# Kernel optimization log

Measured on AMD Instinct MI355X. Metric: run time of the kernel, lower is better.

Reference implementation:

```python
import jax, jax.numpy as jnp
import numpy as np

B, T, D, H, C = 64, 256, 512, 1024, 1000

def setup_inputs() -> dict:
    key = jax.random.key(0)
    ks = jax.random.split(key, 6)
    s = 1.0 / np.sqrt(H)  # torch nn.RNN init scale
    return {
        "x": jax.random.normal(ks[0], (B, T, D), dtype=jnp.float32),
        "w_ih0": jax.random.normal(ks[1], (H, D), dtype=jnp.float32) * s,
        "w_hh0": jax.random.normal(ks[2], (H, H), dtype=jnp.float32) * s,
        "w_ih1": jax.random.normal(ks[3], (H, H), dtype=jnp.float32) * s,
        "w_hh1": jax.random.normal(ks[4], (H, H), dtype=jnp.float32) * s,
        "w_fc": jax.random.normal(ks[5], (C, H), dtype=jnp.float32) * s,
    }

def _rnn_layer(inp, w_ih, w_hh):
    # inp: [B, T, Din]; ReLU RNN, no bias (matches nn.RNN(nonlinearity='relu', bias=False))
    xs = jnp.einsum('btd,hd->tbh', inp, w_ih)  # precompute input projections for all steps
    h0 = jnp.zeros((inp.shape[0], w_hh.shape[0]), dtype=inp.dtype)
    def step(h, x_t):
        h = jax.nn.relu(x_t + h @ w_hh.T)
        return h, h
    _, ys = jax.lax.scan(step, h0, xs)  # ys: [T, B, H]
    return jnp.swapaxes(ys, 0, 1)  # [B, T, H]

def reference(x, w_ih0, w_hh0, w_ih1, w_hh1, w_fc):
    h1 = _rnn_layer(x, w_ih0, w_hh0)
    h2 = _rnn_layer(h1, w_ih1, w_hh1)
    # fc on last timestep, no bias
    return h2[:, -1, :] @ w_fc.T  # [B, C]
```

## Files before the change

### kernel.cpp

```cpp
#include <hip/hip_runtime.h>

#define T_STEPS 256
#define BATCH   64
#define HID     1024
#define DIN     512
#define NCLS    1000
#define NBLK    128
#define HSZ     (BATCH * HID)

typedef __attribute__((ext_vector_type(8))) short  short8;
typedef __attribute__((ext_vector_type(4))) float  f32x4;

__device__ __forceinline__ unsigned short rne_bf16(float f) {
    unsigned int u = __builtin_bit_cast(unsigned int, f);
    u += 0x7FFFu + ((u >> 16) & 1u);
    return (unsigned short)(u >> 16);
}
__device__ __forceinline__ float bf16_to_f(unsigned short h) {
    unsigned int u = ((unsigned int)h) << 16;
    return __builtin_bit_cast(float, u);
}

#define MFMA(a, b, c) __builtin_amdgcn_mfma_f32_16x16x32_bf16((a), (b), (c), 0, 0, 0)

__device__ __forceinline__ void grid_bar(int* cnt, int* gen, int bid, int tid, int p) {
    __syncthreads();
    if (tid == 0) {
        __threadfence();
        __hip_atomic_fetch_add(&cnt[(bid & 7) * 32], 1,
                               __ATOMIC_RELAXED, __HIP_MEMORY_SCOPE_AGENT);
        if (bid == 0) {
            const int target = NBLK * (p + 1);
            for (long it = 0; it < 1000000L; ++it) {
                int s = 0;
#pragma unroll
                for (int i = 0; i < 8; ++i)
                    s += __hip_atomic_load(&cnt[i * 32], __ATOMIC_RELAXED,
                                           __HIP_MEMORY_SCOPE_AGENT);
                if (s >= target) break;
                __builtin_amdgcn_s_sleep(1);
            }
            __threadfence();
            __hip_atomic_store(gen, p + 1, __ATOMIC_RELAXED, __HIP_MEMORY_SCOPE_AGENT);
        } else {
            for (long it = 0; it < 1000000L; ++it) {
                if (__hip_atomic_load(gen, __ATOMIC_RELAXED,
                                      __HIP_MEMORY_SCOPE_AGENT) >= p + 1)
                    break;
                __builtin_amdgcn_s_sleep(1);
            }
            __threadfence();
        }
    }
    __syncthreads();
}

__device__ __forceinline__ void reduce_store(const float* red, int tid,
                                             int mbase, int nbase,
                                             unsigned short* ohi, unsigned short* olo,
                                             float* of, const float* xp) {
    const int m = tid >> 4;
    const int n = (tid * 2) & 31;
    float s0, s1;
    if (xp) {
        float2 xi = *(const float2*)(xp + (size_t)(mbase + m) * HID + nbase + n);
        s0 = xi.x; s1 = xi.y;
    } else { s0 = 0.f; s1 = 0.f; }
#pragma unroll
    for (int ww = 0; ww < 8; ++ww) {
        const float* rp = red + ww * 1088 + m * 34 + n;
        s0 += rp[0];
        s1 += rp[1];
    }
    const float v0 = fmaxf(s0, 0.f), v1 = fmaxf(s1, 0.f);
    const unsigned short h0 = rne_bf16(v0), h1 = rne_bf16(v1);
    const unsigned int hp = (unsigned int)h0 | ((unsigned int)h1 << 16);
    const unsigned int lp = (unsigned int)rne_bf16(v0 - bf16_to_f(h0)) |
                            ((unsigned int)rne_bf16(v1 - bf16_to_f(h1)) << 16);
    const size_t o = (size_t)(mbase + m) * HID + nbase + n;
    *(unsigned int*)(ohi + o) = hp;
    *(unsigned int*)(olo + o) = lp;
    if (of) { float2 f2; f2.x = v0; f2.y = v1; *(float2*)(of + o) = f2; }
}

__global__ __launch_bounds__(512, 2)
void rnn_mfma(const float* __restrict__ xproj,
              const unsigned short* __restrict__ whh0h, const unsigned short* __restrict__ whh0l,
              const unsigned short* __restrict__ wih1h, const unsigned short* __restrict__ wih1l,
              const unsigned short* __restrict__ whh1h, const unsigned short* __restrict__ whh1l,
              unsigned short* h1hi, unsigned short* h1lo,
              unsigned short* h2hi, unsigned short* h2lo,
              float* h2f, int* bar) {
    __shared__ float red[8 * 1088];

    const int bid   = blockIdx.x;
    const int z     = bid >> 6;
    const int r     = bid & 63;
    const int nbase = (r >> 1) * 32;
    const int mbase = (r & 1) * 32;
    const int tid   = threadIdx.x;
    const int w     = tid >> 6;
    const int lane  = tid & 63;
    const int l15   = lane & 15;
    const int kq    = (lane >> 4) * 8;

    int* cnt = bar;
    int* gen = bar + 256;

    if (z == 0) {
        short8 WH[2][4], WL[2][4];
        const int kb = w * 128;
#pragma unroll
        for (int c = 0; c < 4; ++c)
#pragma unroll
            for (int nt = 0; nt < 2; ++nt) {
                const size_t o = (size_t)(nbase + nt * 16 + l15) * HID + kb + c * 32 + kq;
                WH[nt][c] = *(const short8*)(whh0h + o);
                WL[nt][c] = *(const short8*)(whh0l + o);
            }
        for (int p = 0; p <= T_STEPS; ++p) {
            if (p < T_STEPS) {
                f32x4 acc[2][2] = {};
                const unsigned short* hch = h1hi + (size_t)(p & 1) * HSZ;
                const unsigned short* hcl = h1lo + (size_t)(p & 1) * HSZ;
#pragma unroll
                for (int c = 0; c < 4; ++c) {
                    short8 ah[2], al[2];
#pragma unroll
                    for (int mt = 0; mt < 2; ++mt) {
                        const size_t o = (size_t)(mbase + mt * 16 + l15) * HID + kb + c * 32 + kq;
                        ah[mt] = *(const short8*)(hch + o);
                        al[mt] = *(const short8*)(hcl + o);
                    }
#pragma unroll
                    for (int mt = 0; mt < 2; ++mt)
#pragma unroll
                        for (int nt = 0; nt < 2; ++nt) {
                            acc[mt][nt] = MFMA(ah[mt], WH[nt][c], acc[mt][nt]);
                            acc[mt][nt] = MFMA(al[mt], WH[nt][c], acc[mt][nt]);
                            acc[mt][nt] = MFMA(ah[mt], WL[nt][c], acc[mt][nt]);
                        }
                }
#pragma unroll
                for (int mt = 0; mt < 2; ++mt)
#pragma unroll
                    for (int nt = 0; nt < 2; ++nt)
#pragma unroll
                        for (int i = 0; i < 4; ++i)
                            red[w * 1088 + (mt * 16 + (lane >> 4) * 4 + i) * 34 +
                                nt * 16 + l15] = acc[mt][nt][i];
                __syncthreads();
                const size_t ob = (size_t)((p + 1) & 1) * HSZ;
                reduce_store(red, tid, mbase, nbase, h1hi + ob, h1lo + ob, nullptr,
                             xproj + (size_t)p * BATCH * HID);
            }
            grid_bar(cnt, gen, bid, tid, p);
        }
    } else {
        short8 WH[2][8], WL[2][8];
        const unsigned short* ph = (w < 4) ? wih1h : whh1h;
        const unsigned short* pl = (w < 4) ? wih1l : whh1l;
        const int kb = (w & 3) * 256;
#pragma unroll
        for (int c = 0; c < 8; ++c)
#pragma unroll
            for (int nt = 0; nt < 2; ++nt) {
                const size_t o = (size_t)(nbase + nt * 16 + l15) * HID + kb + c * 32 + kq;
                WH[nt][c] = *(const short8*)(ph + o);
                WL[nt][c] = *(const short8*)(pl + o);
            }
        for (int p = 0; p <= T_STEPS; ++p) {
            if (p >= 1) {
                f32x4 acc[2][2] = {};
                const unsigned short* ash = (w < 4) ? h1hi + (size_t)(p & 1) * HSZ
                                                    : h2hi + (size_t)((p - 1) & 1) * HSZ;
                const unsigned short* asl = (w < 4) ? h1lo + (size_t)(p & 1) * HSZ
                                                    : h2lo + (size_t)((p - 1) & 1) * HSZ;
#pragma unroll
                for (int c = 0; c < 8; ++c) {
                    short8 ah[2], al[2];
#pragma unroll
                    for (int mt = 0; mt < 2; ++mt) {
                        const size_t o = (size_t)(mbase + mt * 16 + l15) * HID + kb + c * 32 + kq;
                        ah[mt] = *(const short8*)(ash + o);
                        al[mt] = *(const short8*)(asl + o);
                    }
#pragma unroll
                    for (int mt = 0; mt < 2; ++mt)
#pragma unroll
                        for (int nt = 0; nt < 2; ++nt) {
                            acc[mt][nt] = MFMA(ah[mt], WH[nt][c], acc[mt][nt]);
                            acc[mt][nt] = MFMA(al[mt], WH[nt][c], acc[mt][nt]);
                            acc[mt][nt] = MFMA(ah[mt], WL[nt][c], acc[mt][nt]);
                        }
                }
#pragma unroll
                for (int mt = 0; mt < 2; ++mt)
#pragma unroll
                    for (int nt = 0; nt < 2; ++nt)
#pragma unroll
                        for (int i = 0; i < 4; ++i)
                            red[w * 1088 + (mt * 16 + (lane >> 4) * 4 + i) * 34 +
                                nt * 16 + l15] = acc[mt][nt][i];
                __syncthreads();
                const size_t ob = (size_t)(p & 1) * HSZ;
                reduce_store(red, tid, mbase, nbase, h2hi + ob, h2lo + ob,
                             (p == T_STEPS) ? h2f : nullptr, nullptr);
            }
            grid_bar(cnt, gen, bid, tid, p);
        }
    }
}

__global__ __launch_bounds__(512)
void xproj_gemm(const float* __restrict__ x,
                const unsigned short* __restrict__ wh,
                const unsigned short* __restrict__ wl,
                float* __restrict__ xproj) {
    const int t    = blockIdx.x;
    const int nq   = blockIdx.y;
    const int w    = threadIdx.x >> 6;
    const int lane = threadIdx.x & 63;
    const int l15  = lane & 15;
    const int kq   = (lane >> 4) * 8;
    const int n0   = nq * 256 + w * 32;

    f32x4 acc[4][2] = {};
    for (int c = 0; c < 16; ++c) {
        const int k = c * 32 + kq;
        short8 wfh[2], wfl[2];
#pragma unroll
        for (int nt = 0; nt < 2; ++nt) {
            const size_t o = (size_t)(n0 + nt * 16 + l15) * DIN + k;
            wfh[nt] = *(const short8*)(wh + o);
            wfl[nt] = *(const short8*)(wl + o);
        }
#pragma unroll
        for (int mt = 0; mt < 4; ++mt) {
            const float* xr = x + ((size_t)(mt * 16 + l15) * T_STEPS + t) * DIN + k;
            float4 a0 = *(const float4*)xr;
            float4 a1 = *(const float4*)(xr + 4);
            float f[8] = {a0.x, a0.y, a0.z, a0.w, a1.x, a1.y, a1.z, a1.w};
            short8 ah, al;
#pragma unroll
            for (int i = 0; i < 8; ++i) {
                unsigned short h = rne_bf16(f[i]);
                ah[i] = (short)h;
                al[i] = (short)rne_bf16(f[i] - bf16_to_f(h));
            }
#pragma unroll
            for (int nt = 0; nt < 2; ++nt) {
                acc[mt][nt] = MFMA(ah, wfh[nt], acc[mt][nt]);
                acc[mt][nt] = MFMA(al, wfh[nt], acc[mt][nt]);
                acc[mt][nt] = MFMA(ah, wfl[nt], acc[mt][nt]);
            }
        }
    }
    float* op = xproj + (size_t)t * BATCH * HID;
#pragma unroll
    for (int mt = 0; mt < 4; ++mt)
#pragma unroll
        for (int nt = 0; nt < 2; ++nt)
#pragma unroll
            for (int i = 0; i < 4; ++i) {
                const int m = mt * 16 + (lane >> 4) * 4 + i;
                const int n = n0 + nt * 16 + l15;
                op[(size_t)m * HID + n] = acc[mt][nt][i];
            }
}

__global__ void split_w(const float* __restrict__ src,
                        unsigned short* __restrict__ hi,
                        unsigned short* __restrict__ lo, int n) {
    int i = blockIdx.x * 256 + threadIdx.x;
    if (i < n) {
        float v = src[i];
        unsigned short h = rne_bf16(v);
        hi[i] = h;
        lo[i] = rne_bf16(v - bf16_to_f(h));
    }
}

__global__ void zero_kernel(int* __restrict__ p, int n) {
    int i = blockIdx.x * 256 + threadIdx.x;
    if (i < n) p[i] = 0;
}

__global__ void fc_kernel(const float* __restrict__ h2,
                          const float* __restrict__ w_fc,
                          float* __restrict__ out) {
    __shared__ float hs[HID];
    const int b = blockIdx.x;
    for (int i = threadIdx.x; i < HID; i += 256) hs[i] = h2[(size_t)b * HID + i];
    __syncthreads();
    const int c = blockIdx.y * 256 + threadIdx.x;
    if (c < NCLS) {
        const float* w = w_fc + (size_t)c * HID;
        float s = 0.f;
        for (int k = 0; k < HID; k += 4) {
            float4 wv = *(const float4*)(w + k);
            s += wv.x * hs[k] + wv.y * hs[k + 1] + wv.z * hs[k + 2] + wv.w * hs[k + 3];
        }
        out[(size_t)b * NCLS + c] = s;
    }
}

extern "C" void kernel_launch(void* const* d_in, const int* in_sizes, int n_in,
                              void* d_out, int out_size, void* d_ws, size_t ws_size,
                              hipStream_t stream) {
    const float* x     = (const float*)d_in[0];
    const float* w_ih0 = (const float*)d_in[1];
    const float* w_hh0 = (const float*)d_in[2];
    const float* w_ih1 = (const float*)d_in[3];
    const float* w_hh1 = (const float*)d_in[4];
    const float* w_fc  = (const float*)d_in[5];
    float* out = (float*)d_out;

    char* ws = (char*)d_ws;
    size_t off = 0;
    auto alloc = [&](size_t bytes) { char* p = ws + off; off += bytes; return p; };
    float*          xproj = (float*)alloc((size_t)T_STEPS * BATCH * HID * 4);
    unsigned short* wih0h = (unsigned short*)alloc((size_t)DIN * HID * 2);
    unsigned short* wih0l = (unsigned short*)alloc((size_t)DIN * HID * 2);
    unsigned short* whh0h = (unsigned short*)alloc((size_t)HID * HID * 2);
    unsigned short* whh0l = (unsigned short*)alloc((size_t)HID * HID * 2);
    unsigned short* wih1h = (unsigned short*)alloc((size_t)HID * HID * 2);
    unsigned short* wih1l = (unsigned short*)alloc((size_t)HID * HID * 2);
    unsigned short* whh1h = (unsigned short*)alloc((size_t)HID * HID * 2);
    unsigned short* whh1l = (unsigned short*)alloc((size_t)HID * HID * 2);
    unsigned short* h1hi  = (unsigned short*)alloc(2 * HSZ * 2);
    unsigned short* h1lo  = (unsigned short*)alloc(2 * HSZ * 2);
    unsigned short* h2hi  = (unsigned short*)alloc(2 * HSZ * 2);
    unsigned short* h2lo  = (unsigned short*)alloc(2 * HSZ * 2);
    float*          h2f   = (float*)alloc(HSZ * 4);
    int*            bar   = (int*)alloc(4096);

    split_w<<<(DIN * HID + 255) / 256, 256, 0, stream>>>(w_ih0, wih0h, wih0l, DIN * HID);
    split_w<<<(HID * HID + 255) / 256, 256, 0, stream>>>(w_hh0, whh0h, whh0l, HID * HID);
    split_w<<<(HID * HID + 255) / 256, 256, 0, stream>>>(w_ih1, wih1h, wih1l, HID * HID);
    split_w<<<(HID * HID + 255) / 256, 256, 0, stream>>>(w_hh1, whh1h, whh1l, HID * HID);

    xproj_gemm<<<dim3(T_STEPS, 4), 512, 0, stream>>>(x, wih0h, wih0l, xproj);

    const int nzero = (4 * (2 * HSZ * 2) + HSZ * 4 + 4096) / 4;
    zero_kernel<<<(nzero + 255) / 256, 256, 0, stream>>>((int*)h1hi, nzero);

    rnn_mfma<<<NBLK, 512, 0, stream>>>(xproj,
                                       whh0h, whh0l,
                                       wih1h, wih1l, whh1h, whh1l,
                                       h1hi, h1lo, h2hi, h2lo, h2f, bar);

    fc_kernel<<<dim3(64, 4), 256, 0, stream>>>(h2f, w_fc, out);
}
```

Measured before the change: 4.005 ms.

## Split grid barrier by batch half and replace fences with agent-scope atomic accesses

The grid barrier is split into two independent groups of 64 blocks keyed on the batch half, since each batch half's recurrence depends only on its own rows. The centralized master/generation-flag barrier is replaced by a flat one: every block increments a counter, then spins on the summed counters without sleeping. Thread fences are dropped; hidden-state stores and loads become relaxed agent-scope atomics so the data bypasses non-coherent caches. This is meant to cut per-step barrier latency over 257 steps, but it relies on relaxed ordering without fences and adds more polling traffic.

```diff
diff --git a/kernel.cpp b/kernel.cpp
--- a/kernel.cpp
+++ b/kernel.cpp
@@ -10,6 +10,7 @@
 
 typedef __attribute__((ext_vector_type(8))) short  short8;
 typedef __attribute__((ext_vector_type(4))) float  f32x4;
+typedef unsigned long long u64;
 
 __device__ __forceinline__ unsigned short rne_bf16(float f) {
     unsigned int u = __builtin_bit_cast(unsigned int, f);
@@ -23,34 +24,32 @@
 
 #define MFMA(a, b, c) __builtin_amdgcn_mfma_f32_16x16x32_bf16((a), (b), (c), 0, 0, 0)
 
-__device__ __forceinline__ void grid_bar(int* cnt, int* gen, int bid, int tid, int p) {
+__device__ __forceinline__ short8 ld_st8(const unsigned short* p) {
+    u64 a = __hip_atomic_load((const u64*)p,       __ATOMIC_RELAXED, __HIP_MEMORY_SCOPE_AGENT);
+    u64 b = __hip_atomic_load((const u64*)(p + 4), __ATOMIC_RELAXED, __HIP_MEMORY_SCOPE_AGENT);
+    union { u64 q[2]; short8 v; } u;
+    u.q[0] = a; u.q[1] = b;
+    return u.v;
+}
+__device__ __forceinline__ void st_u32(unsigned short* p, unsigned int v) {
+    __hip_atomic_store((unsigned int*)p, v, __ATOMIC_RELAXED, __HIP_MEMORY_SCOPE_AGENT);
+}
+
+__device__ __forceinline__ void grid_bar(int* cnt, int bid, int tid, int p) {
     __syncthreads();
     if (tid == 0) {
-        __threadfence();
-        __hip_atomic_fetch_add(&cnt[(bid & 7) * 32], 1,
+        __hip_atomic_fetch_add(&cnt[((bid >> 1) & 7) * 32], 1,
                                __ATOMIC_RELAXED, __HIP_MEMORY_SCOPE_AGENT);
-        if (bid == 0) {
-            const int target = NBLK * (p + 1);
-            for (long it = 0; it < 1000000L; ++it) {
-                int s = 0;
-#pragma unroll
-                for (int i = 0; i < 8; ++i)
-                    s += __hip_atomic_load(&cnt[i * 32], __ATOMIC_RELAXED,
-                                           __HIP_MEMORY_SCOPE_AGENT);
-                if (s >= target) break;
-                __builtin_amdgcn_s_sleep(1);
-            }
-            __threadfence();
-            __hip_atomic_store(gen, p + 1, __ATOMIC_RELAXED, __HIP_MEMORY_SCOPE_AGENT);
-        } else {
-            for (long it = 0; it < 1000000L; ++it) {
-                if (__hip_atomic_load(gen, __ATOMIC_RELAXED,
-                                      __HIP_MEMORY_SCOPE_AGENT) >= p + 1)
-                    break;
-                __builtin_amdgcn_s_sleep(1);
-            }
-            __threadfence();
-        }
+        const int target = 64 * (p + 1);
+        for (long it = 0; it < 50000000L; ++it) {
+            int s = 0;
+#pragma unroll
+            for (int i = 0; i < 8; ++i)
+                s += __hip_atomic_load(&cnt[i * 32], __ATOMIC_RELAXED,
+                                       __HIP_MEMORY_SCOPE_AGENT);
+            if (s >= target) break;
+        }
+        asm volatile("" ::: "memory");
     }
     __syncthreads();
 }
@@ -78,8 +77,8 @@
     const unsigned int lp = (unsigned int)rne_bf16(v0 - bf16_to_f(h0)) |
                             ((unsigned int)rne_bf16(v1 - bf16_to_f(h1)) << 16);
     const size_t o = (size_t)(mbase + m) * HID + nbase + n;
-    *(unsigned int*)(ohi + o) = hp;
-    *(unsigned int*)(olo + o) = lp;
+    st_u32(ohi + o, hp);
+    st_u32(olo + o, lp);
     if (of) { float2 f2; f2.x = v0; f2.y = v1; *(float2*)(of + o) = f2; }
 }
 
@@ -104,8 +103,7 @@
     const int l15   = lane & 15;
     const int kq    = (lane >> 4) * 8;
 
-    int* cnt = bar;
-    int* gen = bar + 256;
+    int* cnt = bar + (bid & 1) * 256;
 
     if (z == 0) {
         short8 WH[2][4], WL[2][4];
@@ -129,8 +127,8 @@
 #pragma unroll
                     for (int mt = 0; mt < 2; ++mt) {
                         const size_t o = (size_t)(mbase + mt * 16 + l15) * HID + kb + c * 32 + kq;
-                        ah[mt] = *(const short8*)(hch + o);
-                        al[mt] = *(const short8*)(hcl + o);
+                        ah[mt] = ld_st8(hch + o);
+                        al[mt] = ld_st8(hcl + o);
                     }
 #pragma unroll
                     for (int mt = 0; mt < 2; ++mt)
@@ -154,7 +152,7 @@
                 reduce_store(red, tid, mbase, nbase, h1hi + ob, h1lo + ob, nullptr,
                              xproj + (size_t)p * BATCH * HID);
             }
-            grid_bar(cnt, gen, bid, tid, p);
+            grid_bar(cnt, bid, tid, p);
         }
     } else {
         short8 WH[2][8], WL[2][8];
@@ -182,8 +180,8 @@
 #pragma unroll
                     for (int mt = 0; mt < 2; ++mt) {
                         const size_t o = (size_t)(mbase + mt * 16 + l15) * HID + kb + c * 32 + kq;
-                        ah[mt] = *(const short8*)(ash + o);
-                        al[mt] = *(const short8*)(asl + o);
+                        ah[mt] = ld_st8(ash + o);
+                        al[mt] = ld_st8(asl + o);
                     }
 #pragma unroll
                     for (int mt = 0; mt < 2; ++mt)
@@ -207,7 +205,7 @@
                 reduce_store(red, tid, mbase, nbase, h2hi + ob, h2lo + ob,
                              (p == T_STEPS) ? h2f : nullptr, nullptr);
             }
-            grid_bar(cnt, gen, bid, tid, p);
+            grid_bar(cnt, bid, tid, p);
         }
     }
 }
```

Result: slower. 4.445 ms (+11.0%).
